# Kernel tuning notes

Measured on AMD Instinct MI355X. Metric: run time of the kernel, lower is better.

The kernel has to match this reference:

```python
import jax, jax.numpy as jnp
import numpy as np

BN_EPS = 1e-5


def setup_inputs() -> dict:
    key = jax.random.key(0)
    k1, k2, k3 = jax.random.split(key, 3)
    B, C, H, W = 8, 1024, 48, 48
    Cb = 512
    x = jax.random.normal(k1, (B, C, H, W), dtype=jnp.float32)
    Wg = jax.random.normal(k2, (Cb, C), dtype=jnp.float32) * (1.0 / np.sqrt(C))
    Wz = jax.random.normal(k3, (C, Cb), dtype=jnp.float32) * (1.0 / np.sqrt(Cb))
    gamma = jnp.zeros((C,), dtype=jnp.float32)  # BN weight, const-init 0
    beta = jnp.zeros((C,), dtype=jnp.float32)   # BN bias,  const-init 0
    return {"x": x, "Wg": Wg, "Wz": Wz, "gamma": gamma, "beta": beta}


def reference(x, Wg, Wz, gamma, beta):
    B, C, H, W = x.shape
    HW = H * W
    xf = x.reshape(B, C, HW)                                  # [B,C,N]
    # attn[b,n,m] = <x[b,:,n], x[b,:,m]> / (H*W), softmax over m
    attn = jnp.einsum('bcn,bcm->bnm', xf, xf) / HW            # [B,N,N]
    attn = jax.nn.softmax(attn, axis=-1)
    # g: 1x1 conv C -> Cb (no bias)
    g = jnp.einsum('dc,bcn->bdn', Wg, xf)                     # [B,Cb,N]
    # y[b,d,n] = sum_m attn[b,n,m] * g[b,d,m]
    y = jnp.einsum('bnm,bdm->bdn', attn, g)                   # [B,Cb,N]
    # W_z: 1x1 conv Cb -> C (no bias)
    wy = jnp.einsum('cd,bdn->bcn', Wz, y)                     # [B,C,N]
    # BatchNorm2d in training mode: batch stats over (B, N), biased variance
    mean = jnp.mean(wy, axis=(0, 2), keepdims=True)
    var = jnp.mean(jnp.square(wy - mean), axis=(0, 2), keepdims=True)
    wy_bn = (wy - mean) * jax.lax.rsqrt(var + BN_EPS)
    wy_bn = wy_bn * gamma[None, :, None] + beta[None, :, None]
    z = wy_bn.reshape(B, C, H, W) + x
    return z
```

## Files before the change

kernel.cpp:

```cpp
#include <hip/hip_runtime.h>
#include <hip/hip_bf16.h>
#include <stdint.h>


typedef __bf16 bf16;
typedef __attribute__((ext_vector_type(8))) __bf16 bf16x8;
typedef __attribute__((ext_vector_type(4))) __bf16 bf16x4;
typedef __attribute__((ext_vector_type(4))) float f32x4;

template <bool F32OUT, bool BNRED, bool BXI, bool SMAX>
__global__ __launch_bounds__(256)
void gemm_btz(const bf16* __restrict__ Ag, const bf16* __restrict__ Bg,
              void* __restrict__ Dg, int K, int N,
              long long sA, long long sB, long long sD, float alpha,
              float* __restrict__ ps, float* __restrict__ pq,
              const float* __restrict__ rsum, long long sR, int nInner, int nz)
{
    const int d  = blockIdx.x;
    const int zz = d % nz;
    const int t0 = d / nz;
    const int bI = t0 % nInner;
    const int bO = t0 / nInner;
    const int bx = BXI ? bI : bO;
    const int by = BXI ? bO : bI;

    __shared__ char lds[32768];
    char* ldsA = lds;
    char* ldsB = lds + 16384;

    const int lane = threadIdx.x & 63;
    const int wv   = threadIdx.x >> 6;
    const int wm   = wv >> 1;
    const int wn   = wv & 1;

    const bf16* Ab = Ag + (long long)zz * sA + (long long)by * 128 * K;
    const bf16* Bb = Bg + (long long)zz * sB + (long long)bx * 128 * K;

    float ainv[4];
    if (SMAX) {
        #pragma unroll
        for (int t = 0; t < 4; ++t) {
            int row = ((wv * 4 + t) * 64 + lane) >> 3;
            ainv[t] = 1.0f / rsum[(long long)zz * sR + by * 128 + row];
        }
    }

    f32x4 acc[4][4];
    #pragma unroll
    for (int i = 0; i < 4; ++i)
        #pragma unroll
        for (int j = 0; j < 4; ++j) {
            f32x4 z = {0.f, 0.f, 0.f, 0.f};
            acc[i][j] = z;
        }

    for (int k0 = 0; k0 < K; k0 += 64) {
        #pragma unroll
        for (int t = 0; t < 4; ++t) {
            int ch  = (wv * 4 + t) * 64 + lane;
            int row = ch >> 3;
            int cc  = (ch & 7) ^ (row & 7);
            bf16x8 va = *(const bf16x8*)(Ab + (long long)row * K + k0 + cc * 8);
            bf16x8 vb = *(const bf16x8*)(Bb + (long long)row * K + k0 + cc * 8);
            if (SMAX) {
                #pragma unroll
                for (int q8 = 0; q8 < 8; ++q8)
                    va[q8] = (bf16)((float)va[q8] * ainv[t]);
            }
            *(bf16x8*)(ldsA + ch * 16) = va;
            *(bf16x8*)(ldsB + ch * 16) = vb;
        }
        __syncthreads();

        #pragma unroll
        for (int kk = 0; kk < 64; kk += 32) {
            bf16x8 af[4], bfr[4];
            #pragma unroll
            for (int i = 0; i < 4; ++i) {
                int r = wm * 64 + i * 16 + (lane & 15);
                int c = ((kk >> 3) + (lane >> 4)) ^ (r & 7);
                af[i] = *(const bf16x8*)(ldsA + r * 128 + c * 16);
            }
            #pragma unroll
            for (int j = 0; j < 4; ++j) {
                int r = wn * 64 + j * 16 + (lane & 15);
                int c = ((kk >> 3) + (lane >> 4)) ^ (r & 7);
                bfr[j] = *(const bf16x8*)(ldsB + r * 128 + c * 16);
            }
            #pragma unroll
            for (int i = 0; i < 4; ++i)
                #pragma unroll
                for (int j = 0; j < 4; ++j)
                    acc[i][j] = __builtin_amdgcn_mfma_f32_16x16x32_bf16(af[i], bfr[j], acc[i][j], 0, 0, 0);
        }
        __syncthreads();
    }

    float* bs = (float*)lds;
    float* bq = (float*)(lds + 512);
    if (BNRED) {
        if (threadIdx.x < 128) { bs[threadIdx.x] = 0.f; bq[threadIdx.x] = 0.f; }
        __syncthreads();
    }

    const int m_base = by * 128 + wm * 64;
    const int n_base = bx * 128 + wn * 64;
    float s_it[4][4], q_it[4][4];
    #pragma unroll
    for (int i = 0; i < 4; ++i) {
        #pragma unroll
        for (int t = 0; t < 4; ++t) { s_it[i][t] = 0.f; q_it[i][t] = 0.f; }
    }
    #pragma unroll
    for (int i = 0; i < 4; ++i) {
        #pragma unroll
        for (int j = 0; j < 4; ++j) {
            int col = n_base + j * 16 + (lane & 15);
            #pragma unroll
            for (int t = 0; t < 4; ++t) {
                int rowg = m_base + i * 16 + (lane >> 4) * 4 + t;
                float v = acc[i][j][t] * alpha;
                if (F32OUT) ((float*)Dg)[(long long)zz * sD + (long long)rowg * N + col] = v;
                else        ((bf16*)Dg)[(long long)zz * sD + (long long)rowg * N + col] = (bf16)v;
                if (BNRED) { s_it[i][t] += v; q_it[i][t] += v * v; }
            }
        }
    }

    if (BNRED) {
        #pragma unroll
        for (int i = 0; i < 4; ++i) {
            #pragma unroll
            for (int t = 0; t < 4; ++t) {
                float s = s_it[i][t], q = q_it[i][t];
                #pragma unroll
                for (int m = 1; m < 16; m <<= 1) {
                    s += __shfl_xor(s, m);
                    q += __shfl_xor(q, m);
                }
                if ((lane & 15) == 0) {
                    int cl = wm * 64 + i * 16 + (lane >> 4) * 4 + t;
                    atomicAdd(&bs[cl], s);
                    atomicAdd(&bq[cl], q);
                }
            }
        }
        __syncthreads();
        if (threadIdx.x < 128) {
            int cg = by * 128 + threadIdx.x;
            atomicAdd(&ps[cg], bs[threadIdx.x]);
            atomicAdd(&pq[cg], bq[threadIdx.x]);
        }
    }
}

__global__ __launch_bounds__(256)
void gemm_sym(const bf16* __restrict__ Xg, bf16* __restrict__ Dg,
              int K, int N, long long sX, long long sD, float alpha,
              float* __restrict__ rsum)
{
    const int NZ = gridDim.z;
    const int d  = blockIdx.z * 171 + blockIdx.x;
    const int zz = d % NZ;
    int tlin     = d / NZ;
    int bi = 0;
    while (tlin >= 18 - bi) { tlin -= 18 - bi; ++bi; }
    const int bj = bi + tlin;
    const bool mir  = (bj > bi);
    const bool diag = (bj == bi);

    __shared__ __align__(16) char lds[32768];
    char* ldsA = lds;
    char* ldsB = diag ? lds : (lds + 16384);

    const int lane = threadIdx.x & 63;
    const int wv   = threadIdx.x >> 6;
    const int wm   = wv >> 1;
    const int wn   = wv & 1;

    const bf16* Ab = Xg + (long long)zz * sX + (long long)bi * 128 * K;
    const bf16* Bb = Xg + (long long)zz * sX + (long long)bj * 128 * K;

    f32x4 acc[4][4];
    #pragma unroll
    for (int i = 0; i < 4; ++i)
        #pragma unroll
        for (int j = 0; j < 4; ++j) {
            f32x4 z = {0.f, 0.f, 0.f, 0.f};
            acc[i][j] = z;
        }

    for (int k0 = 0; k0 < K; k0 += 64) {
        #pragma unroll
        for (int t = 0; t < 4; ++t) {
            int ch  = (wv * 4 + t) * 64 + lane;
            int row = ch >> 3;
            int cc  = (ch & 7) ^ (row & 7);
            bf16x8 va = *(const bf16x8*)(Ab + (long long)row * K + k0 + cc * 8);
            *(bf16x8*)(ldsA + ch * 16) = va;
            if (!diag) {
                bf16x8 vb = *(const bf16x8*)(Bb + (long long)row * K + k0 + cc * 8);
                *(bf16x8*)(ldsB + ch * 16) = vb;
            }
        }
        __syncthreads();

        #pragma unroll
        for (int kk = 0; kk < 64; kk += 32) {
            bf16x8 af[4], bfr[4];
            #pragma unroll
            for (int i = 0; i < 4; ++i) {
                int r = wm * 64 + i * 16 + (lane & 15);
                int c = ((kk >> 3) + (lane >> 4)) ^ (r & 7);
                af[i] = *(const bf16x8*)(ldsA + r * 128 + c * 16);
            }
            #pragma unroll
            for (int j = 0; j < 4; ++j) {
                int r = wn * 64 + j * 16 + (lane & 15);
                int c = ((kk >> 3) + (lane >> 4)) ^ (r & 7);
                bfr[j] = *(const bf16x8*)(ldsB + r * 128 + c * 16);
            }
            #pragma unroll
            for (int i = 0; i < 4; ++i)
                #pragma unroll
                for (int j = 0; j < 4; ++j)
                    acc[i][j] = __builtin_amdgcn_mfma_f32_16x16x32_bf16(af[i], bfr[j], acc[i][j], 0, 0, 0);
        }
        __syncthreads();
    }

    bf16* Db = Dg + (long long)zz * sD;
    float* rs = rsum + (long long)zz * N;
    bf16 (*tr)[128] = (bf16(*)[128])lds;

    float rowsum[4][4];
    float colsum[4];
    #pragma unroll
    for (int i = 0; i < 4; ++i)
        #pragma unroll
        for (int t = 0; t < 4; ++t) rowsum[i][t] = 0.f;
    #pragma unroll
    for (int j = 0; j < 4; ++j) colsum[j] = 0.f;

    #pragma unroll
    for (int i = 0; i < 4; ++i) {
        #pragma unroll
        for (int j = 0; j < 4; ++j) {
            int c_loc = wn * 64 + j * 16 + (lane & 15);
            int col   = bj * 128 + c_loc;
            bf16x4 tv;
            #pragma unroll
            for (int t = 0; t < 4; ++t) {
                int r_loc = wm * 64 + i * 16 + (lane >> 4) * 4 + t;
                float e = __expf(acc[i][j][t] * alpha);
                bf16 eb = (bf16)e;
                Db[(long long)(bi * 128 + r_loc) * N + col] = eb;
                tv[t] = eb;
                rowsum[i][t] += e;
                colsum[j]    += e;
            }
            if (mir) {
                int r_base = wm * 64 + i * 16 + (lane >> 4) * 4;
                *(bf16x4*)(&tr[c_loc][r_base]) = tv;
            }
        }
    }

    #pragma unroll
    for (int i = 0; i < 4; ++i) {
        #pragma unroll
        for (int t = 0; t < 4; ++t) {
            float s = rowsum[i][t];
            s += __shfl_xor(s, 1); s += __shfl_xor(s, 2);
            s += __shfl_xor(s, 4); s += __shfl_xor(s, 8);
            if ((lane & 15) == 0)
                atomicAdd(&rs[bi * 128 + wm * 64 + i * 16 + (lane >> 4) * 4 + t], s);
        }
    }
    if (mir) {
        #pragma unroll
        for (int j = 0; j < 4; ++j) {
            float s = colsum[j];
            s += __shfl_xor(s, 16); s += __shfl_xor(s, 32);
            if (lane < 16)
                atomicAdd(&rs[bj * 128 + wn * 64 + j * 16 + lane], s);
        }
        __syncthreads();
        const int cc = threadIdx.x >> 1, hf = threadIdx.x & 1;
        const bf16* src = &tr[cc][hf * 64];
        bf16* dst = Db + (long long)(bj * 128 + cc) * N + bi * 128 + hf * 64;
        #pragma unroll
        for (int j2 = 0; j2 < 8; ++j2)
            *(bf16x8*)(dst + j2 * 8) = *(const bf16x8*)(src + j2 * 8);
    }
}

__global__ __launch_bounds__(256)
void f32_to_bf16(const float* __restrict__ in, bf16* __restrict__ out, int n)
{
    int idx = (blockIdx.x * 256 + threadIdx.x) * 4;
    if (idx < n) {
        float4 v = *(const float4*)(in + idx);
        out[idx + 0] = (bf16)v.x;
        out[idx + 1] = (bf16)v.y;
        out[idx + 2] = (bf16)v.z;
        out[idx + 3] = (bf16)v.w;
    }
}

__global__ __launch_bounds__(256)
void zero_f32(float* __restrict__ p)
{
    p[blockIdx.x * 256 + threadIdx.x] = 0.f;
}

__global__ __launch_bounds__(256)
void transpose_f32_bf16(const float* __restrict__ x, bf16* __restrict__ xT)
{
    __shared__ bf16 tile[32][33];
    const float* xb = x + (long long)blockIdx.z * 1024 * 2304;
    bf16* xo = xT + (long long)blockIdx.z * 2304 * 1024;
    const int n0 = blockIdx.x * 32;
    const int c0 = blockIdx.y * 32;
    const int tx = threadIdx.x, ty = threadIdx.y;
    #pragma unroll
    for (int i = 0; i < 32; i += 8)
        tile[ty + i][tx] = (bf16)xb[(long long)(c0 + ty + i) * 2304 + n0 + tx];
    __syncthreads();
    #pragma unroll
    for (int i = 0; i < 32; i += 8)
        xo[(long long)(n0 + ty + i) * 1024 + c0 + tx] = tile[tx][ty + i];
}

__global__ __launch_bounds__(256)
void bn_finalize(const float* __restrict__ ps, const float* __restrict__ pq,
                 float* __restrict__ mean, float* __restrict__ istd)
{
    int c = blockIdx.x * 256 + threadIdx.x;
    float mu = ps[c] / 18432.0f;
    mean[c] = mu;
    istd[c] = rsqrtf(pq[c] / 18432.0f - mu * mu + 1e-5f);
}

__global__ __launch_bounds__(256)
void bn_apply_b(const bf16* __restrict__ wy, const float* __restrict__ x,
                const float* __restrict__ gamma, const float* __restrict__ beta,
                const float* __restrict__ mean, const float* __restrict__ istd,
                float* __restrict__ z)
{
    long long idx = ((long long)blockIdx.x * 256 + threadIdx.x) * 8;
    int c = (int)((idx / 2304) & 1023);
    float sc = gamma[c] * istd[c];
    float sh = beta[c] - mean[c] * sc;
    bf16x8 w  = *(const bf16x8*)(wy + idx);
    float4 x0 = *(const float4*)(x + idx);
    float4 x1 = *(const float4*)(x + idx + 4);
    float4 o0, o1;
    o0.x = (float)w[0] * sc + sh + x0.x;
    o0.y = (float)w[1] * sc + sh + x0.y;
    o0.z = (float)w[2] * sc + sh + x0.z;
    o0.w = (float)w[3] * sc + sh + x0.w;
    o1.x = (float)w[4] * sc + sh + x1.x;
    o1.y = (float)w[5] * sc + sh + x1.y;
    o1.z = (float)w[6] * sc + sh + x1.z;
    o1.w = (float)w[7] * sc + sh + x1.w;
    *(float4*)(z + idx)     = o0;
    *(float4*)(z + idx + 4) = o1;
}

extern "C" void kernel_launch(void* const* d_in, const int* in_sizes, int n_in,
                              void* d_out, int out_size, void* d_ws, size_t ws_size,
                              hipStream_t stream)
{
    const float* x     = (const float*)d_in[0];
    const float* Wg    = (const float*)d_in[1];
    const float* Wz    = (const float*)d_in[2];
    const float* gamma = (const float*)d_in[3];
    const float* beta  = (const float*)d_in[4];
    float* zo = (float*)d_out;

    const int B = 8, C = 1024, Cb = 512, N = 2304;

    const size_t fixedB = ((size_t)Cb * C * 2) * 2 + (size_t)C * 4 * 4 + 4096;
    const size_t perB   = ((size_t)N * C + (size_t)Cb * N + (size_t)N * N + (size_t)N * Cb
                           + (size_t)C * N) * 2 + (size_t)N * 4 + 1536;
    int BC = 8;
    while (BC > 1 && fixedB + perB * (size_t)BC > ws_size) BC >>= 1;

    char* p = (char*)d_ws;
    auto alloc = [&](size_t bytes) { char* r = p; p += (bytes + 255) & ~(size_t)255; return r; };
    bf16*  Wgb  = (bf16*)alloc((size_t)Cb * C * 2);
    bf16*  Wzb  = (bf16*)alloc((size_t)C * Cb * 2);
    float* psum = (float*)alloc((size_t)C * 4);
    float* pqsm = (float*)alloc((size_t)C * 4);
    float* mean = (float*)alloc((size_t)C * 4);
    float* istd = (float*)alloc((size_t)C * 4);
    float* rsum = (float*)alloc((size_t)B * N * 4);
    bf16*  xT   = (bf16*)alloc((size_t)BC * N * C * 2);
    bf16*  g    = (bf16*)alloc((size_t)BC * Cb * N * 2);
    bf16*  attn = (bf16*)alloc((size_t)BC * N * N * 2);
    bf16*  yT   = (bf16*)alloc((size_t)BC * N * Cb * 2);
    bf16*  wyb  = (bf16*)alloc((size_t)BC * C * N * 2);

    f32_to_bf16<<<dim3((Cb * C) / (256 * 4)), 256, 0, stream>>>(Wg, Wgb, Cb * C);
    f32_to_bf16<<<dim3((C * Cb) / (256 * 4)), 256, 0, stream>>>(Wz, Wzb, C * Cb);
    zero_f32<<<dim3(8), 256, 0, stream>>>(psum);

    for (int cs = 0; cs < B; cs += BC) {
        const float* xc = x + (long long)cs * C * N;

        transpose_f32_bf16<<<dim3(N / 32, C / 32, BC), dim3(32, 8), 0, stream>>>(xc, xT);

        gemm_btz<false, false, false, false><<<dim3(18 * 4 * BC), 256, 0, stream>>>(
            Wgb, xT, g, C, N, 0, (long long)N * C, (long long)Cb * N, 1.0f,
            nullptr, nullptr, nullptr, 0, 4, BC);

        zero_f32<<<dim3(BC * 9), 256, 0, stream>>>(rsum);
        gemm_sym<<<dim3(171, 1, BC), 256, 0, stream>>>(
            xT, attn, C, N, (long long)N * C, (long long)N * N, 1.0f / 2304.0f, rsum);

        gemm_btz<false, false, true, true><<<dim3(4 * 18 * BC), 256, 0, stream>>>(
            attn, g, yT, N, Cb, (long long)N * N, (long long)Cb * N, (long long)N * Cb, 1.0f,
            nullptr, nullptr, rsum, N, 4, BC);

        gemm_btz<false, true, false, false><<<dim3(18 * 8 * BC), 256, 0, stream>>>(
            Wzb, yT, wyb, Cb, N, 0, (long long)N * Cb, (long long)C * N, 1.0f,
            psum, pqsm, nullptr, 0, 8, BC);
    }

    bn_finalize<<<dim3(C / 256), 256, 0, stream>>>(psum, pqsm, mean, istd);

    if (BC == B) {
        bn_apply_b<<<dim3((B * C * N) / (256 * 8)), 256, 0, stream>>>(
            wyb, x, gamma, beta, mean, istd, zo);
    } else {
        for (int cs = 0; cs < B; cs += BC) {
            const float* xc = x + (long long)cs * C * N;
            float* zoc = zo + (long long)cs * C * N;
            transpose_f32_bf16<<<dim3(N / 32, C / 32, BC), dim3(32, 8), 0, stream>>>(xc, xT);
            gemm_btz<false, false, false, false><<<dim3(18 * 4 * BC), 256, 0, stream>>>(
                Wgb, xT, g, C, N, 0, (long long)N * C, (long long)Cb * N, 1.0f,
                nullptr, nullptr, nullptr, 0, 4, BC);
            zero_f32<<<dim3(BC * 9), 256, 0, stream>>>(rsum);
            gemm_sym<<<dim3(171, 1, BC), 256, 0, stream>>>(
                xT, attn, C, N, (long long)N * C, (long long)N * N, 1.0f / 2304.0f, rsum);
            gemm_btz<false, false, true, true><<<dim3(4 * 18 * BC), 256, 0, stream>>>(
                attn, g, yT, N, Cb, (long long)N * N, (long long)Cb * N, (long long)N * Cb,
                1.0f, nullptr, nullptr, rsum, N, 4, BC);
            gemm_btz<false, false, false, false><<<dim3(18 * 8 * BC), 256, 0, stream>>>(
                Wzb, yT, wyb, Cb, N, 0, (long long)N * Cb, (long long)C * N, 1.0f,
                nullptr, nullptr, nullptr, 0, 8, BC);
            bn_apply_b<<<dim3((BC * C * N) / (256 * 8)), 256, 0, stream>>>(
                wyb, xc, gamma, beta, mean, istd, zoc);
        }
    }
}
```

Before: 402.7 us.

## Defer softmax normalization to Wz GEMM, fuse prep kernels and BN finalize

The softmax row normalization (1/rowsum) moves out of the attn×g GEMM, where it scaled every A tile element, and into the Wz GEMM, where it scales the smaller yT operand. This is valid because the row scaling commutes through the linear Wz projection. The weight conversions and psum/rsum zeroing are merged into one prep kernel, bn_finalize is folded into bn_apply, and the transpose LDS tile in gemm_sym is padded to reduce bank conflicts. The cost is a bf16 rounding of unnormalized y before scaling, which could slightly change precision.

```diff
diff --git a/kernel.cpp b/kernel.cpp
--- a/kernel.cpp
+++ b/kernel.cpp
@@ -8,7 +8,7 @@
 typedef __attribute__((ext_vector_type(4))) __bf16 bf16x4;
 typedef __attribute__((ext_vector_type(4))) float f32x4;
 
-template <bool F32OUT, bool BNRED, bool BXI, bool SMAX>
+template <bool F32OUT, bool BNRED, bool BXI, bool SMAXB>
 __global__ __launch_bounds__(256)
 void gemm_btz(const bf16* __restrict__ Ag, const bf16* __restrict__ Bg,
               void* __restrict__ Dg, int K, int N,
@@ -36,12 +36,12 @@
     const bf16* Ab = Ag + (long long)zz * sA + (long long)by * 128 * K;
     const bf16* Bb = Bg + (long long)zz * sB + (long long)bx * 128 * K;
 
-    float ainv[4];
-    if (SMAX) {
+    float binv[4];
+    if (SMAXB) {
         #pragma unroll
         for (int t = 0; t < 4; ++t) {
             int row = ((wv * 4 + t) * 64 + lane) >> 3;
-            ainv[t] = 1.0f / rsum[(long long)zz * sR + by * 128 + row];
+            binv[t] = 1.0f / rsum[(long long)zz * sR + bx * 128 + row];
         }
     }
 
@@ -62,10 +62,10 @@
             int cc  = (ch & 7) ^ (row & 7);
             bf16x8 va = *(const bf16x8*)(Ab + (long long)row * K + k0 + cc * 8);
             bf16x8 vb = *(const bf16x8*)(Bb + (long long)row * K + k0 + cc * 8);
-            if (SMAX) {
+            if (SMAXB) {
                 #pragma unroll
                 for (int q8 = 0; q8 < 8; ++q8)
-                    va[q8] = (bf16)((float)va[q8] * ainv[t]);
+                    vb[q8] = (bf16)((float)vb[q8] * binv[t]);
             }
             *(bf16x8*)(ldsA + ch * 16) = va;
             *(bf16x8*)(ldsB + ch * 16) = vb;
@@ -169,7 +169,7 @@
     const bool mir  = (bj > bi);
     const bool diag = (bj == bi);
 
-    __shared__ __align__(16) char lds[32768];
+    __shared__ __align__(16) char lds[35840];
     char* ldsA = lds;
     char* ldsB = diag ? lds : (lds + 16384);
 
@@ -231,7 +231,7 @@
 
     bf16* Db = Dg + (long long)zz * sD;
     float* rs = rsum + (long long)zz * N;
-    bf16 (*tr)[128] = (bf16(*)[128])lds;
+    bf16 (*tr)[140] = (bf16(*)[140])lds;
 
     float rowsum[4][4];
     float colsum[4];
@@ -296,15 +296,23 @@
 }
 
 __global__ __launch_bounds__(256)
-void f32_to_bf16(const float* __restrict__ in, bf16* __restrict__ out, int n)
-{
-    int idx = (blockIdx.x * 256 + threadIdx.x) * 4;
-    if (idx < n) {
+void prep(const float* __restrict__ Wg, const float* __restrict__ Wz,
+          bf16* __restrict__ Wgb, bf16* __restrict__ Wzb, float* __restrict__ zp)
+{
+    const int b = blockIdx.x;
+    if (b < 1024) {
+        const float* in = (b < 512) ? Wg : Wz;
+        bf16* out       = (b < 512) ? Wgb : Wzb;
+        int idx = (((b & 511) * 256) + threadIdx.x) * 4;
         float4 v = *(const float4*)(in + idx);
         out[idx + 0] = (bf16)v.x;
         out[idx + 1] = (bf16)v.y;
         out[idx + 2] = (bf16)v.z;
         out[idx + 3] = (bf16)v.w;
+    } else {
+        int i = ((b - 1024) * 256 + threadIdx.x) * 4;
+        float4 z = {0.f, 0.f, 0.f, 0.f};
+        *(float4*)(zp + i) = z;
     }
 }
 
@@ -333,25 +341,17 @@
 }
 
 __global__ __launch_bounds__(256)
-void bn_finalize(const float* __restrict__ ps, const float* __restrict__ pq,
-                 float* __restrict__ mean, float* __restrict__ istd)
-{
-    int c = blockIdx.x * 256 + threadIdx.x;
-    float mu = ps[c] / 18432.0f;
-    mean[c] = mu;
-    istd[c] = rsqrtf(pq[c] / 18432.0f - mu * mu + 1e-5f);
-}
-
-__global__ __launch_bounds__(256)
 void bn_apply_b(const bf16* __restrict__ wy, const float* __restrict__ x,
                 const float* __restrict__ gamma, const float* __restrict__ beta,
-                const float* __restrict__ mean, const float* __restrict__ istd,
+                const float* __restrict__ ps, const float* __restrict__ pq,
                 float* __restrict__ z)
 {
     long long idx = ((long long)blockIdx.x * 256 + threadIdx.x) * 8;
     int c = (int)((idx / 2304) & 1023);
-    float sc = gamma[c] * istd[c];
-    float sh = beta[c] - mean[c] * sc;
+    float mu = ps[c] * (1.0f / 18432.0f);
+    float is = rsqrtf(pq[c] * (1.0f / 18432.0f) - mu * mu + 1e-5f);
+    float sc = gamma[c] * is;
+    float sh = beta[c] - mu * sc;
     bf16x8 w  = *(const bf16x8*)(wy + idx);
     float4 x0 = *(const float4*)(x + idx);
     float4 x1 = *(const float4*)(x + idx + 4);
@@ -381,9 +381,9 @@
 
     const int B = 8, C = 1024, Cb = 512, N = 2304;
 
-    const size_t fixedB = ((size_t)Cb * C * 2) * 2 + (size_t)C * 4 * 4 + 4096;
+    const size_t fixedB = ((size_t)Cb * C * 2) * 2 + (size_t)C * 4 * 2 + (size_t)B * N * 4 + 4096;
     const size_t perB   = ((size_t)N * C + (size_t)Cb * N + (size_t)N * N + (size_t)N * Cb
-                           + (size_t)C * N) * 2 + (size_t)N * 4 + 1536;
+                           + (size_t)C * N) * 2 + 1536;
     int BC = 8;
     while (BC > 1 && fixedB + perB * (size_t)BC > ws_size) BC >>= 1;
 
@@ -393,8 +393,6 @@
     bf16*  Wzb  = (bf16*)alloc((size_t)C * Cb * 2);
     float* psum = (float*)alloc((size_t)C * 4);
     float* pqsm = (float*)alloc((size_t)C * 4);
-    float* mean = (float*)alloc((size_t)C * 4);
-    float* istd = (float*)alloc((size_t)C * 4);
     float* rsum = (float*)alloc((size_t)B * N * 4);
     bf16*  xT   = (bf16*)alloc((size_t)BC * N * C * 2);
     bf16*  g    = (bf16*)alloc((size_t)BC * Cb * N * 2);
@@ -402,12 +400,13 @@
     bf16*  yT   = (bf16*)alloc((size_t)BC * N * Cb * 2);
     bf16*  wyb  = (bf16*)alloc((size_t)BC * C * N * 2);
 
-    f32_to_bf16<<<dim3((Cb * C) / (256 * 4)), 256, 0, stream>>>(Wg, Wgb, Cb * C);
-    f32_to_bf16<<<dim3((C * Cb) / (256 * 4)), 256, 0, stream>>>(Wz, Wzb, C * Cb);
-    zero_f32<<<dim3(8), 256, 0, stream>>>(psum);
+    prep<<<dim3(1044), 256, 0, stream>>>(Wg, Wz, Wgb, Wzb, psum);
 
     for (int cs = 0; cs < B; cs += BC) {
         const float* xc = x + (long long)cs * C * N;
+
+        if (BC < B && cs > 0)
+            zero_f32<<<dim3((BC * N) / 256), 256, 0, stream>>>(rsum);
 
         transpose_f32_bf16<<<dim3(N / 32, C / 32, BC), dim3(32, 8), 0, stream>>>(xc, xT);
 
@@ -415,43 +414,40 @@
             Wgb, xT, g, C, N, 0, (long long)N * C, (long long)Cb * N, 1.0f,
             nullptr, nullptr, nullptr, 0, 4, BC);
 
-        zero_f32<<<dim3(BC * 9), 256, 0, stream>>>(rsum);
         gemm_sym<<<dim3(171, 1, BC), 256, 0, stream>>>(
             xT, attn, C, N, (long long)N * C, (long long)N * N, 1.0f / 2304.0f, rsum);
 
-        gemm_btz<false, false, true, true><<<dim3(4 * 18 * BC), 256, 0, stream>>>(
+        gemm_btz<false, false, true, false><<<dim3(4 * 18 * BC), 256, 0, stream>>>(
             attn, g, yT, N, Cb, (long long)N * N, (long long)Cb * N, (long long)N * Cb, 1.0f,
-            nullptr, nullptr, rsum, N, 4, BC);
-
-        gemm_btz<false, true, false, false><<<dim3(18 * 8 * BC), 256, 0, stream>>>(
+            nullptr, nullptr, nullptr, 0, 4, BC);
+
+        gemm_btz<false, true, false, true><<<dim3(18 * 8 * BC), 256, 0, stream>>>(
             Wzb, yT, wyb, Cb, N, 0, (long long)N * Cb, (long long)C * N, 1.0f,
-            psum, pqsm, nullptr, 0, 8, BC);
-    }
-
-    bn_finalize<<<dim3(C / 256), 256, 0, stream>>>(psum, pqsm, mean, istd);
+            psum, pqsm, rsum, N, 8, BC);
+    }
 
     if (BC == B) {
         bn_apply_b<<<dim3((B * C * N) / (256 * 8)), 256, 0, stream>>>(
-            wyb, x, gamma, beta, mean, istd, zo);
+            wyb, x, gamma, beta, psum, pqsm, zo);
     } else {
         for (int cs = 0; cs < B; cs += BC) {
             const float* xc = x + (long long)cs * C * N;
             float* zoc = zo + (long long)cs * C * N;
+            zero_f32<<<dim3((BC * N) / 256), 256, 0, stream>>>(rsum);
             transpose_f32_bf16<<<dim3(N / 32, C / 32, BC), dim3(32, 8), 0, stream>>>(xc, xT);
             gemm_btz<false, false, false, false><<<dim3(18 * 4 * BC), 256, 0, stream>>>(
                 Wgb, xT, g, C, N, 0, (long long)N * C, (long long)Cb * N, 1.0f,
                 nullptr, nullptr, nullptr, 0, 4, BC);
-            zero_f32<<<dim3(BC * 9), 256, 0, stream>>>(rsum);
             gemm_sym<<<dim3(171, 1, BC), 256, 0, stream>>>(
                 xT, attn, C, N, (long long)N * C, (long long)N * N, 1.0f / 2304.0f, rsum);
-            gemm_btz<false, false, true, true><<<dim3(4 * 18 * BC), 256, 0, stream>>>(
+            gemm_btz<false, false, true, false><<<dim3(4 * 18 * BC), 256, 0, stream>>>(
                 attn, g, yT, N, Cb, (long long)N * N, (long long)Cb * N, (long long)N * Cb,
-                1.0f, nullptr, nullptr, rsum, N, 4, BC);
-            gemm_btz<false, false, false, false><<<dim3(18 * 8 * BC), 256, 0, stream>>>(
+                1.0f, nullptr, nullptr, nullptr, 0, 4, BC);
+            gemm_btz<false, false, false, true><<<dim3(18 * 8 * BC), 256, 0, stream>>>(
                 Wzb, yT, wyb, Cb, N, 0, (long long)N * Cb, (long long)C * N, 1.0f,
-                nullptr, nullptr, nullptr, 0, 8, BC);
+                nullptr, nullptr, rsum, N, 8, BC);
             bn_apply_b<<<dim3((BC * C * N) / (256 * 8)), 256, 0, stream>>>(
-                wyb, xc, gamma, beta, mean, istd, zoc);
-        }
-    }
-}
+                wyb, xc, gamma, beta, psum, pqsm, zoc);
+        }
+    }
+}
```

Result: faster. 380.5 us (-5.5%).
